# Kernel optimization log

Measured on AMD Instinct MI355X. Metric: run time of the kernel, lower is better.

## Reference

```python
import jax, jax.numpy as jnp
from jax import lax
import numpy as np

B, C, H, W = 8, 4, 512, 512
SIGMA, W0 = 5.0, 10.0
_DBIG = 1e6  # sentinel 1D distance (larger than any image diagonal)


def setup_inputs() -> dict:
    key = jax.random.key(0)
    k1, k2 = jax.random.split(key)
    pred = jax.random.normal(k1, (B, C, H, W), jnp.float32)
    labels = jax.random.randint(k2, (B, H, W), 0, C)
    target = jax.nn.one_hot(labels, C, axis=1, dtype=jnp.float32)  # (B,C,H,W) one-hot
    return {"pred": pred, "target": target}


def _edt_sq(mask):
    """Exact squared Euclidean distance transform to True pixels of a (H,W) bool mask.
    Equivalent to scipy.ndimage.distance_transform_edt(1 - mask)**2.
    Pass 1: exact 1D distance along axis 1 via forward/backward cummax of feature indices.
    Pass 2: min-plus envelope along axis 0: D2[i,j] = min_k g[k,j]^2 + (i-k)^2."""
    Hh, Ww = mask.shape
    col = jnp.arange(Ww, dtype=jnp.float32)
    # nearest feature index to the left / right within each row
    left = lax.cummax(jnp.where(mask, col, -_DBIG), axis=1)
    dl = col[None, :] - left
    rneg = lax.cummax(jnp.where(mask, -col, -_DBIG), axis=1, reverse=True)
    dr = -rneg - col[None, :]
    g = jnp.minimum(jnp.minimum(dl, dr), _DBIG)  # (H,W) 1D distance
    g2 = g * g
    rows = jnp.arange(Hh, dtype=jnp.float32)

    def step(D2, xs):
        g2k, k = xs  # row k's 1D squared distances
        cand = g2k[None, :] + (rows - k)[:, None] ** 2
        return jnp.minimum(D2, cand), None

    D2, _ = lax.scan(step, jnp.full((Hh, Ww), _DBIG * _DBIG, jnp.float32), (g2, rows))
    return D2


def _border_weights(target, sigma, w0):
    """U-Net border weight map: w = 1 + w0*exp(-(d1+d2)^2 / (2 sigma^2))."""
    label_map = jnp.argmax(target, axis=1)  # (B,H,W)
    Cn = target.shape[1]
    masks = label_map[:, None, :, :] == jnp.arange(Cn)[None, :, None, None]  # (B,C,H,W)
    # a class contributes a distance map only if it has both fg and bg pixels
    valid = masks.any(axis=(2, 3)) & (~masks).any(axis=(2, 3))  # (B,C)
    D2 = jax.vmap(jax.vmap(_edt_sq))(masks)  # (B,C,H,W)
    dist = jnp.where(valid[:, :, None, None], jnp.sqrt(D2), _DBIG)
    ds = jnp.sort(dist, axis=1)  # invalid classes sort to the end (sentinel)
    d1, d2 = ds[:, 0], ds[:, 1]
    # if fewer than 2 valid classes, d2 (and possibly d1) is the sentinel -> exp underflows to 0 -> w == 1,
    # matching the torch code's early-continue (weights stay 1).
    return 1.0 + w0 * jnp.exp(-((d1 + d2) ** 2) / (2.0 * sigma * sigma))


def reference(pred, target):
    logp = jax.nn.log_softmax(pred, axis=1)
    target_idx = jnp.argmax(target, axis=1)  # (B,H,W)
    per_pixel = -jnp.take_along_axis(logp, target_idx[:, None], axis=1)[:, 0]  # CE, reduction='none'
    w = lax.stop_gradient(_border_weights(target, SIGMA, W0))  # weights built from detached target
    weighted = jnp.mean(per_pixel * w)
    base = jnp.mean(-(target * logp).sum(axis=1))  # soft cross-entropy base loss
    return base + weighted
```

## Files before the change

### kernel.cpp

```cpp
#include <hip/hip_runtime.h>
#include <stdint.h>

#define HH 512
#define WW 512
#define CC 4
#define BB 8
#define NPIX (BB * HH * WW)
#define SLAB 8
#define NBLK (BB * HH / SLAB)

__device__ __forceinline__ float row_min_sq(uint32_t v) {
    float c0 = (float)(v & 255u);
    float c1 = (float)((v >> 8) & 255u);
    float c2 = (float)((v >> 16) & 255u);
    float c3 = (float)(v >> 24);
    return fminf(fminf(c0 * c0, c1 * c1), fminf(c2 * c2, c3 * c3));
}

__device__ __forceinline__ uint32_t own_mask(uint32_t v) {
    uint32_t z = (~((v & 0x7F7F7F7Fu) + 0x7F7F7F7Fu)) & ~v & 0x80808080u;
    return (z >> 7) * 255u;
}

__device__ __forceinline__ void scan_row(const float* __restrict__ trow,
                                         int lane, uint32_t* __restrict__ ldsrow) {
    const int j0 = lane << 3;
    const size_t CH = (size_t)HH * WW;

    int L[8];
    {
        const float4* p0 = reinterpret_cast<const float4*>(trow + j0);
        const float4* p1 = reinterpret_cast<const float4*>(trow + CH + j0);
        const float4* p2 = reinterpret_cast<const float4*>(trow + 2 * CH + j0);
        float4 a0 = p0[0], b0 = p0[1];
        float4 a1 = p1[0], b1 = p1[1];
        float4 a2 = p2[0], b2 = p2[1];
        float t0[8] = {a0.x, a0.y, a0.z, a0.w, b0.x, b0.y, b0.z, b0.w};
        float t1[8] = {a1.x, a1.y, a1.z, a1.w, b1.x, b1.y, b1.z, b1.w};
        float t2[8] = {a2.x, a2.y, a2.z, a2.w, b2.x, b2.y, b2.z, b2.w};
        #pragma unroll
        for (int jj = 0; jj < 8; ++jj)
            L[jj] = (t0[jj] == 1.0f) ? 0 : (t1[jj] == 1.0f) ? 1 : (t2[jj] == 1.0f) ? 2 : 3;
    }

    uint32_t gp[8] = {0, 0, 0, 0, 0, 0, 0, 0};
    #pragma unroll
    for (int c = 0; c < CC; ++c) {
        int run = -1000000;
        int lastL[8];
        #pragma unroll
        for (int jj = 0; jj < 8; ++jj) { if (L[jj] == c) run = j0 + jj; lastL[jj] = run; }
        int incl = run;
        #pragma unroll
        for (int d = 1; d < 64; d <<= 1) {
            int up = __shfl_up(incl, (unsigned)d, 64);
            if (lane >= d) incl = max(incl, up);
        }
        int excl = __shfl_up(incl, 1u, 64);
        if (lane == 0) excl = -1000000;

        int nrun = 1000000;
        int nxtL[8];
        #pragma unroll
        for (int jj = 7; jj >= 0; --jj) { if (L[jj] == c) nrun = j0 + jj; nxtL[jj] = nrun; }
        int rincl = nrun;
        #pragma unroll
        for (int d = 1; d < 64; d <<= 1) {
            int dn = __shfl_down(rincl, (unsigned)d, 64);
            if (lane < 64 - d) rincl = min(rincl, dn);
        }
        int rexcl = __shfl_down(rincl, 1u, 64);
        if (lane == 63) rexcl = 1000000;

        #pragma unroll
        for (int jj = 0; jj < 8; ++jj) {
            int last = max(lastL[jj], excl);
            int nxt  = min(nxtL[jj], rexcl);
            int gg = min(min((j0 + jj) - last, nxt - (j0 + jj)), 255);
            gp[jj] |= ((uint32_t)gg) << (c * 8);
        }
    }
    uint4* o = reinterpret_cast<uint4*>(ldsrow + j0);
    o[0] = make_uint4(gp[0], gp[1], gp[2], gp[3]);
    o[1] = make_uint4(gp[4], gp[5], gp[6], gp[7]);
}

__global__ __launch_bounds__(512, 4) void k_fused(const float* __restrict__ pred,
                                                  const float* __restrict__ target,
                                                  float* __restrict__ partial) {
    __shared__ uint32_t gl[12][WW];
    __shared__ float red[8];
    __shared__ int sflag;

    const int bid0 = blockIdx.x;
    const int bid = ((bid0 & 7) << 6) | (bid0 >> 3);
    const int b  = bid >> 6;
    const int i0 = (bid & 63) << 3;
    const int tid = threadIdx.x, wid = tid >> 6, lane = tid & 63;
    const size_t CH = (size_t)HH * WW;
    const float* tbase = target + (size_t)b * CC * CH;

    const int rp = tid >> 7;
    const int s0 = rp << 1;
    const int j4 = (tid & 127) << 2;
    float4 pA[CC], pB[CC];
    {
        const float* pbase = pred + ((size_t)b * CC * HH + (size_t)i0) * WW + j4;
        #pragma unroll
        for (int c = 0; c < CC; ++c) {
            pA[c] = *reinterpret_cast<const float4*>(pbase + ((size_t)c * HH + s0) * WW);
            pB[c] = *reinterpret_cast<const float4*>(pbase + ((size_t)c * HH + s0 + 1) * WW);
        }
    }

    {
        int r = i0 - 2 + wid;
        if (r >= 0 && r < HH) scan_row(tbase + (size_t)r * WW, lane, gl[wid]);
        if (wid < 4) {
            int r2 = i0 + 6 + wid;
            if (r2 < HH) scan_row(tbase + (size_t)r2 * WW, lane, gl[8 + wid]);
        }
    }
    if (tid == 0) sflag = 0;
    __syncthreads();

    uint4 vv[6];
    #pragma unroll
    for (int t = 0; t < 6; ++t) vv[t] = *reinterpret_cast<const uint4*>(&gl[s0 + t][j4]);

    uint32_t om0[4], om1[4];
    float b0[4], b1[4];
    {
        uint32_t w0[4] = {vv[2].x, vv[2].y, vv[2].z, vv[2].w};
        uint32_t w1[4] = {vv[3].x, vv[3].y, vv[3].z, vv[3].w};
        #pragma unroll
        for (int x = 0; x < 4; ++x) {
            om0[x] = own_mask(w0[x]); b0[x] = row_min_sq(w0[x] | om0[x]);
            om1[x] = own_mask(w1[x]); b1[x] = row_min_sq(w1[x] | om1[x]);
        }
    }
    #pragma unroll
    for (int dk = -2; dk <= 2; ++dk) {
        if (dk == 0) continue;
        const float dk2 = (float)(dk * dk);
        if ((unsigned)(i0 + s0 + dk) < (unsigned)HH) {
            const uint4 v = vv[2 + dk];
            uint32_t w[4] = {v.x, v.y, v.z, v.w};
            #pragma unroll
            for (int x = 0; x < 4; ++x) b0[x] = fminf(b0[x], row_min_sq(w[x] | om0[x]) + dk2);
        }
        if ((unsigned)(i0 + s0 + 1 + dk) < (unsigned)HH) {
            const uint4 v = vv[3 + dk];
            uint32_t w[4] = {v.x, v.y, v.z, v.w};
            #pragma unroll
            for (int x = 0; x < 4; ++x) b1[x] = fminf(b1[x], row_min_sq(w[x] | om1[x]) + dk2);
        }
    }

    {
        float mx = 0.f;
        #pragma unroll
        for (int x = 0; x < 4; ++x) mx = fmaxf(mx, fmaxf(b0[x], b1[x]));
        if (__any(mx > 9.0f)) { if (lane == 0) sflag = 1; }
    }
    __syncthreads();

    if (sflag) {
        for (int dk = 3; dk < HH; ++dk) {
            { int rr = i0 + wid - dk;
              if (rr >= 0 && rr < HH) scan_row(tbase + (size_t)rr * WW, lane, gl[wid]); }
            __syncthreads();
            const float dk2 = (float)(dk * dk);
            if (i0 + s0 - dk >= 0) {
                uint4 v = *reinterpret_cast<const uint4*>(&gl[s0][j4]);
                uint32_t w[4] = {v.x, v.y, v.z, v.w};
                #pragma unroll
                for (int x = 0; x < 4; ++x) b0[x] = fminf(b0[x], row_min_sq(w[x] | om0[x]) + dk2);
            }
            if (i0 + s0 + 1 - dk >= 0) {
                uint4 v = *reinterpret_cast<const uint4*>(&gl[s0 + 1][j4]);
                uint32_t w[4] = {v.x, v.y, v.z, v.w};
                #pragma unroll
                for (int x = 0; x < 4; ++x) b1[x] = fminf(b1[x], row_min_sq(w[x] | om1[x]) + dk2);
            }
            __syncthreads();
            { int rr = i0 + wid + dk;
              if (rr < HH) scan_row(tbase + (size_t)rr * WW, lane, gl[wid]); }
            __syncthreads();
            if (i0 + s0 + dk < HH) {
                uint4 v = *reinterpret_cast<const uint4*>(&gl[s0][j4]);
                uint32_t w[4] = {v.x, v.y, v.z, v.w};
                #pragma unroll
                for (int x = 0; x < 4; ++x) b0[x] = fminf(b0[x], row_min_sq(w[x] | om0[x]) + dk2);
            }
            if (i0 + s0 + 1 + dk < HH) {
                uint4 v = *reinterpret_cast<const uint4*>(&gl[s0 + 1][j4]);
                uint32_t w[4] = {v.x, v.y, v.z, v.w};
                #pragma unroll
                for (int x = 0; x < 4; ++x) b1[x] = fminf(b1[x], row_min_sq(w[x] | om1[x]) + dk2);
            }
            __syncthreads();
            if (tid == 0) sflag = 0;
            __syncthreads();
            const float nthr = (float)((dk + 1) * (dk + 1));
            float mx = 0.f;
            #pragma unroll
            for (int x = 0; x < 4; ++x) mx = fmaxf(mx, fmaxf(b0[x], b1[x]));
            if (__any(mx > nthr)) { if (lane == 0) sflag = 1; }
            __syncthreads();
            if (!sflag) break;
            if (i0 + SLAB - 1 - dk < 0 && i0 + dk >= HH) break;
        }
    }

    float vacc = 0.f;
    #pragma unroll
    for (int x = 0; x < 4; ++x) {
        {
            float a[CC] = {reinterpret_cast<const float*>(&pA[0])[x],
                           reinterpret_cast<const float*>(&pA[1])[x],
                           reinterpret_cast<const float*>(&pA[2])[x],
                           reinterpret_cast<const float*>(&pA[3])[x]};
            const int L = __builtin_ctz(om0[x]) >> 3;
            float m = fmaxf(fmaxf(a[0], a[1]), fmaxf(a[2], a[3]));
            float ssum = __expf(a[0] - m) + __expf(a[1] - m) +
                         __expf(a[2] - m) + __expf(a[3] - m);
            float xs = (L == 0) ? a[0] : (L == 1) ? a[1] : (L == 2) ? a[2] : a[3];
            float pp = (m + __logf(ssum)) - xs;
            vacc += pp * fmaf(10.0f, __expf(-0.02f * b0[x]), 2.0f);
        }
        {
            float a[CC] = {reinterpret_cast<const float*>(&pB[0])[x],
                           reinterpret_cast<const float*>(&pB[1])[x],
                           reinterpret_cast<const float*>(&pB[2])[x],
                           reinterpret_cast<const float*>(&pB[3])[x]};
            const int L = __builtin_ctz(om1[x]) >> 3;
            float m = fmaxf(fmaxf(a[0], a[1]), fmaxf(a[2], a[3]));
            float ssum = __expf(a[0] - m) + __expf(a[1] - m) +
                         __expf(a[2] - m) + __expf(a[3] - m);
            float xs = (L == 0) ? a[0] : (L == 1) ? a[1] : (L == 2) ? a[2] : a[3];
            float pp = (m + __logf(ssum)) - xs;
            vacc += pp * fmaf(10.0f, __expf(-0.02f * b1[x]), 2.0f);
        }
    }

    #pragma unroll
    for (int off = 32; off > 0; off >>= 1) vacc += __shfl_down(vacc, (unsigned)off, 64);
    if (lane == 0) red[wid] = vacc;
    __syncthreads();
    if (tid == 0) {
        float bsum = ((red[0] + red[1]) + (red[2] + red[3]))
                   + ((red[4] + red[5]) + (red[6] + red[7]));
        partial[blockIdx.x] = bsum;
    }
}

__global__ __launch_bounds__(256) void k_red(const float* __restrict__ partial,
                                             float* __restrict__ out) {
    __shared__ double sd[256];
    double a = (double)partial[threadIdx.x] + (double)partial[threadIdx.x + 256];
    sd[threadIdx.x] = a;
    __syncthreads();
    #pragma unroll
    for (int s = 128; s > 0; s >>= 1) {
        if (threadIdx.x < s) sd[threadIdx.x] += sd[threadIdx.x + s];
        __syncthreads();
    }
    if (threadIdx.x == 0) out[0] = (float)(sd[0] * (1.0 / (double)NPIX));
}

extern "C" void kernel_launch(void* const* d_in, const int* in_sizes, int n_in,
                              void* d_out, int out_size, void* d_ws, size_t ws_size,
                              hipStream_t stream) {
    const float* pred   = (const float*)d_in[0];
    const float* target = (const float*)d_in[1];
    float* partial = (float*)d_ws;
    float* out = (float*)d_out;

    hipLaunchKernelGGL(k_fused, dim3(NBLK), dim3(512), 0, stream, pred, target, partial);
    hipLaunchKernelGGL(k_red, dim3(1), dim3(256), 0, stream, partial, out);
}
```

Measured before the change: 27.69 us.

## Compute per-pixel cross-entropy inside row scan and stage it in LDS

Moves the log-softmax and cross-entropy computation for each of the block's own rows into the target row-scan routine, which already holds the label per pixel. Each result is written to a new shared-memory array and read back at the end. This removes the long-lived pred registers that were loaded up front and held across the distance search. The launch-bounds occupancy hint is dropped and about 16KB of LDS is added, which could change occupancy and moves the pred loads onto the critical path before the first barrier.

```diff
diff --git a/kernel.cpp b/kernel.cpp
--- a/kernel.cpp
+++ b/kernel.cpp
@@ -23,7 +23,10 @@
 }
 
 __device__ __forceinline__ void scan_row(const float* __restrict__ trow,
-                                         int lane, uint32_t* __restrict__ ldsrow) {
+                                         const float* __restrict__ prow,
+                                         int lane,
+                                         uint32_t* __restrict__ ldsrow,
+                                         float* __restrict__ pprow) {
     const int j0 = lane << 3;
     const size_t CH = (size_t)HH * WW;
 
@@ -83,12 +86,37 @@
     uint4* o = reinterpret_cast<uint4*>(ldsrow + j0);
     o[0] = make_uint4(gp[0], gp[1], gp[2], gp[3]);
     o[1] = make_uint4(gp[4], gp[5], gp[6], gp[7]);
-}
-
-__global__ __launch_bounds__(512, 4) void k_fused(const float* __restrict__ pred,
-                                                  const float* __restrict__ target,
-                                                  float* __restrict__ partial) {
+
+    if (prow) {
+        float x[CC][8];
+        #pragma unroll
+        for (int c = 0; c < CC; ++c) {
+            const float4* p = reinterpret_cast<const float4*>(prow + (size_t)c * CH + j0);
+            float4 a0 = p[0], a1 = p[1];
+            x[c][0] = a0.x; x[c][1] = a0.y; x[c][2] = a0.z; x[c][3] = a0.w;
+            x[c][4] = a1.x; x[c][5] = a1.y; x[c][6] = a1.z; x[c][7] = a1.w;
+        }
+        float ppv[8];
+        #pragma unroll
+        for (int jj = 0; jj < 8; ++jj) {
+            float m = fmaxf(fmaxf(x[0][jj], x[1][jj]), fmaxf(x[2][jj], x[3][jj]));
+            float s = __expf(x[0][jj] - m) + __expf(x[1][jj] - m) +
+                      __expf(x[2][jj] - m) + __expf(x[3][jj] - m);
+            float xs = (L[jj] == 0) ? x[0][jj] : (L[jj] == 1) ? x[1][jj]
+                     : (L[jj] == 2) ? x[2][jj] : x[3][jj];
+            ppv[jj] = (m + __logf(s)) - xs;
+        }
+        float4* po = reinterpret_cast<float4*>(pprow + j0);
+        po[0] = make_float4(ppv[0], ppv[1], ppv[2], ppv[3]);
+        po[1] = make_float4(ppv[4], ppv[5], ppv[6], ppv[7]);
+    }
+}
+
+__global__ __launch_bounds__(512) void k_fused(const float* __restrict__ pred,
+                                               const float* __restrict__ target,
+                                               float* __restrict__ partial) {
     __shared__ uint32_t gl[12][WW];
+    __shared__ float ppl[8][WW];
     __shared__ float red[8];
     __shared__ int sflag;
 
@@ -99,30 +127,30 @@
     const int tid = threadIdx.x, wid = tid >> 6, lane = tid & 63;
     const size_t CH = (size_t)HH * WW;
     const float* tbase = target + (size_t)b * CC * CH;
+    const float* pbase = pred   + (size_t)b * CC * CH;
+
+    {
+        int r = i0 - 2 + wid;
+        if (r >= 0 && r < HH) {
+            bool ce = (wid >= 2);
+            scan_row(tbase + (size_t)r * WW, ce ? pbase + (size_t)r * WW : nullptr,
+                     lane, gl[wid], ce ? ppl[wid - 2] : nullptr);
+        }
+        if (wid < 4) {
+            int r2 = i0 + 6 + wid;
+            if (r2 < HH) {
+                bool ce = (wid < 2);
+                scan_row(tbase + (size_t)r2 * WW, ce ? pbase + (size_t)r2 * WW : nullptr,
+                         lane, gl[8 + wid], ce ? ppl[6 + wid] : nullptr);
+            }
+        }
+    }
+    if (tid == 0) sflag = 0;
+    __syncthreads();
 
     const int rp = tid >> 7;
     const int s0 = rp << 1;
     const int j4 = (tid & 127) << 2;
-    float4 pA[CC], pB[CC];
-    {
-        const float* pbase = pred + ((size_t)b * CC * HH + (size_t)i0) * WW + j4;
-        #pragma unroll
-        for (int c = 0; c < CC; ++c) {
-            pA[c] = *reinterpret_cast<const float4*>(pbase + ((size_t)c * HH + s0) * WW);
-            pB[c] = *reinterpret_cast<const float4*>(pbase + ((size_t)c * HH + s0 + 1) * WW);
-        }
-    }
-
-    {
-        int r = i0 - 2 + wid;
-        if (r >= 0 && r < HH) scan_row(tbase + (size_t)r * WW, lane, gl[wid]);
-        if (wid < 4) {
-            int r2 = i0 + 6 + wid;
-            if (r2 < HH) scan_row(tbase + (size_t)r2 * WW, lane, gl[8 + wid]);
-        }
-    }
-    if (tid == 0) sflag = 0;
-    __syncthreads();
 
     uint4 vv[6];
     #pragma unroll
@@ -168,7 +196,8 @@
     if (sflag) {
         for (int dk = 3; dk < HH; ++dk) {
             { int rr = i0 + wid - dk;
-              if (rr >= 0 && rr < HH) scan_row(tbase + (size_t)rr * WW, lane, gl[wid]); }
+              if (rr >= 0 && rr < HH)
+                  scan_row(tbase + (size_t)rr * WW, nullptr, lane, gl[wid], nullptr); }
             __syncthreads();
             const float dk2 = (float)(dk * dk);
             if (i0 + s0 - dk >= 0) {
@@ -185,7 +214,8 @@
             }
             __syncthreads();
             { int rr = i0 + wid + dk;
-              if (rr < HH) scan_row(tbase + (size_t)rr * WW, lane, gl[wid]); }
+              if (rr < HH)
+                  scan_row(tbase + (size_t)rr * WW, nullptr, lane, gl[wid], nullptr); }
             __syncthreads();
             if (i0 + s0 + dk < HH) {
                 uint4 v = *reinterpret_cast<const uint4*>(&gl[s0][j4]);
@@ -213,35 +243,15 @@
         }
     }
 
+    float4 ppA = *reinterpret_cast<const float4*>(&ppl[s0][j4]);
+    float4 ppB = *reinterpret_cast<const float4*>(&ppl[s0 + 1][j4]);
+    const float pa[4] = {ppA.x, ppA.y, ppA.z, ppA.w};
+    const float pb[4] = {ppB.x, ppB.y, ppB.z, ppB.w};
     float vacc = 0.f;
     #pragma unroll
     for (int x = 0; x < 4; ++x) {
-        {
-            float a[CC] = {reinterpret_cast<const float*>(&pA[0])[x],
-                           reinterpret_cast<const float*>(&pA[1])[x],
-                           reinterpret_cast<const float*>(&pA[2])[x],
-                           reinterpret_cast<const float*>(&pA[3])[x]};
-            const int L = __builtin_ctz(om0[x]) >> 3;
-            float m = fmaxf(fmaxf(a[0], a[1]), fmaxf(a[2], a[3]));
-            float ssum = __expf(a[0] - m) + __expf(a[1] - m) +
-                         __expf(a[2] - m) + __expf(a[3] - m);
-            float xs = (L == 0) ? a[0] : (L == 1) ? a[1] : (L == 2) ? a[2] : a[3];
-            float pp = (m + __logf(ssum)) - xs;
-            vacc += pp * fmaf(10.0f, __expf(-0.02f * b0[x]), 2.0f);
-        }
-        {
-            float a[CC] = {reinterpret_cast<const float*>(&pB[0])[x],
-                           reinterpret_cast<const float*>(&pB[1])[x],
-                           reinterpret_cast<const float*>(&pB[2])[x],
-                           reinterpret_cast<const float*>(&pB[3])[x]};
-            const int L = __builtin_ctz(om1[x]) >> 3;
-            float m = fmaxf(fmaxf(a[0], a[1]), fmaxf(a[2], a[3]));
-            float ssum = __expf(a[0] - m) + __expf(a[1] - m) +
-                         __expf(a[2] - m) + __expf(a[3] - m);
-            float xs = (L == 0) ? a[0] : (L == 1) ? a[1] : (L == 2) ? a[2] : a[3];
-            float pp = (m + __logf(ssum)) - xs;
-            vacc += pp * fmaf(10.0f, __expf(-0.02f * b1[x]), 2.0f);
-        }
+        vacc += pa[x] * fmaf(10.0f, __expf(-0.02f * b0[x]), 2.0f);
+        vacc += pb[x] * fmaf(10.0f, __expf(-0.02f * b1[x]), 2.0f);
     }
 
     #pragma unroll
```

Result: faster. 25.47 us (median of 2 runs) (-8.0%).
